# Performance work log

Hardware: AMD Instinct MI355X
Metric: run time of the kernel (lower is better)

Reference implementation:

```python
import jax, jax.numpy as jnp
import numpy as np

N_NODES = 100000
N_EDGES = 1600000
F_IN = 128
HID = 64
HORIZON = 100
NUM_TARGETS = 3


def setup_inputs() -> dict:
    key = jax.random.key(0)
    ks = jax.random.split(key, 7)
    x = jax.random.normal(ks[0], (N_NODES, F_IN), dtype=jnp.float32)
    edge_index = jax.random.randint(ks[1], (2, N_EDGES), 0, N_NODES, dtype=jnp.int64)
    s = 1.0 / np.sqrt(F_IN)
    W_l = jax.random.uniform(ks[2], (HID, F_IN), jnp.float32, -s, s)
    b_l = jax.random.uniform(ks[3], (HID,), jnp.float32, -s, s)
    W_r = jax.random.uniform(ks[4], (HID, F_IN), jnp.float32, -s, s)
    s2 = 1.0 / np.sqrt(HID)
    W_out = jax.random.uniform(ks[5], (NUM_TARGETS * HORIZON, HID), jnp.float32, -s2, s2)
    b_out = jax.random.uniform(ks[6], (NUM_TARGETS * HORIZON,), jnp.float32, -s2, s2)
    return {"x": x, "edge_index": edge_index, "W_l": W_l, "b_l": b_l,
            "W_r": W_r, "W_out": W_out, "b_out": b_out}


def reference(x, edge_index, W_l, b_l, W_r, W_out, b_out):
    n = x.shape[0]
    src, dst = edge_index[0], edge_index[1]
    # gather neighbor features and mean-aggregate per destination node
    msgs = x[src]  # [E, F_IN]
    agg = jax.ops.segment_sum(msgs, dst, num_segments=n)  # [N, F_IN]
    cnt = jax.ops.segment_sum(jnp.ones((edge_index.shape[1],), x.dtype), dst, num_segments=n)
    mean = agg / jnp.maximum(cnt, 1.0)[:, None]
    # SAGEConv: lin_l(aggregated) + lin_r(root), bias only on lin_l
    h = jnp.einsum('nf,hf->nh', mean, W_l) + b_l + jnp.einsum('nf,hf->nh', x, W_r)
    h = jax.nn.relu(h)
    out = jnp.einsum('nh,oh->no', h, W_out) + b_out  # [N, NUM_TARGETS*HORIZON]
    return out.reshape(-1, HORIZON)
```

## Files before the change

### kernel.cpp

```cpp
#include <hip/hip_runtime.h>

#define N_NODES 100000
#define F_IN 128
#define HID 64
#define OUT_F 300
#define WO_ROWS 320
#define NBKT 782
#define ECAP 2688
#define PART_BLOCKS 256
#define GEMM_BLOCKS 196
#define SORT_CAP 6400

typedef short bf8 __attribute__((ext_vector_type(8)));
typedef float f32x4 __attribute__((ext_vector_type(4)));

__device__ inline unsigned short f2bf(float f) {
    unsigned u = __builtin_bit_cast(unsigned, f);
    u += 0x7fff + ((u >> 16) & 1);
    return (unsigned short)(u >> 16);
}
__device__ inline float b2f(unsigned short h) {
    return __builtin_bit_cast(float, (unsigned)h << 16);
}

__global__ void k_prep(const float* __restrict__ Wl, const float* __restrict__ Wr,
                       const float* __restrict__ Wout,
                       unsigned short* __restrict__ Wc, unsigned short* __restrict__ Wo,
                       int* __restrict__ gcur) {
    int idx = blockIdx.x * blockDim.x + threadIdx.x;
    if (idx < 128 * 128) {
        int c = idx >> 7, k = idx & 127;
        float v = (c < HID) ? Wl[c * F_IN + k] : Wr[(c - HID) * F_IN + k];
        Wc[idx] = f2bf(v);
    } else if (idx < 128 * 128 + WO_ROWS * HID) {
        int j = idx - 128 * 128;
        int o = j >> 6, k = j & 63;
        Wo[j] = (o < OUT_F) ? f2bf(Wout[o * HID + k]) : (unsigned short)0;
    } else {
        int b = idx - 128 * 128 - WO_ROWS * HID;
        if (b < NBKT) gcur[b] = 0;
    }
}

__global__ __launch_bounds__(512) void k_pg(const int* __restrict__ ei,
                                            int* __restrict__ gcur,
                                            unsigned* __restrict__ pedges, int nE,
                                            const float* __restrict__ x,
                                            const unsigned short* __restrict__ Wc,
                                            unsigned short* __restrict__ yz) {
    if (blockIdx.x < PART_BLOCKS) {
        __shared__ unsigned sorted[SORT_CAP];
        __shared__ int hcnt[1024], hoff[1024], hcur[1024];
        __shared__ int wpre[8];
        const int tid = threadIdx.x, lane = tid & 63, wid = tid >> 6;
        const int per = (nE + PART_BLOCKS - 1) / PART_BLOCKS;
        const int e0 = blockIdx.x * per;
        const int e1 = min(e0 + per, nE);
        for (int cb = e0; cb < e1; cb += SORT_CAP) {
            const int cnt = min(SORT_CAP, e1 - cb);
            hcnt[tid * 2] = 0; hcnt[tid * 2 + 1] = 0;
            __syncthreads();
            for (int i = tid; i < cnt; i += 512)
                atomicAdd(&hcnt[ei[nE + cb + i] >> 7], 1);
            __syncthreads();
            int c0 = hcnt[tid * 2], c1 = hcnt[tid * 2 + 1];
            int tsum = c0 + c1;
            int s = tsum;
#pragma unroll
            for (int d = 1; d < 64; d <<= 1) { int t = __shfl_up(s, d, 64); if (lane >= d) s += t; }
            if (lane == 63) wpre[wid] = s;
            __syncthreads();
            if (tid == 0) { int run = 0; for (int w = 0; w < 8; ++w) { int t = wpre[w]; wpre[w] = run; run += t; } }
            __syncthreads();
            int excl = wpre[wid] + (s - tsum);
            hoff[tid * 2 + 0] = excl;       hcur[tid * 2 + 0] = excl;
            hoff[tid * 2 + 1] = excl + c0;  hcur[tid * 2 + 1] = excl + c0;
            __syncthreads();
            for (int i = tid; i < cnt; i += 512) {
                int src = ei[cb + i];
                int dst = ei[nE + cb + i];
                unsigned pk = ((unsigned)src << 7) | (unsigned)(dst & 127);
                int p = atomicAdd(&hcur[dst >> 7], 1);
                sorted[p] = pk;
            }
            __syncthreads();
            for (int b = tid; b < NBKT; b += 512) {
                int c = hcnt[b];
                if (c > 0) {
                    int gp = atomicAdd(&gcur[b], c);
                    unsigned* dst = pedges + (size_t)b * ECAP + gp;
                    int off = hoff[b];
                    for (int i = 0; i < c; ++i) dst[i] = sorted[off + i];
                }
            }
            __syncthreads();
        }
    } else {
        const int wv = threadIdx.x >> 6;
        const int nb = (blockIdx.x - PART_BLOCKS) * 512 + wv * 64;
        if (nb >= N_NODES) return;
        const int lane = threadIdx.x & 63;
        const int lm = lane & 15, lk = lane >> 4;

        f32x4 acc[4][8];
#pragma unroll
        for (int a = 0; a < 4; ++a)
#pragma unroll
            for (int b = 0; b < 8; ++b) acc[a][b] = f32x4{0.f, 0.f, 0.f, 0.f};

#pragma unroll
        for (int kt = 0; kt < 4; ++kt) {
            const int ko = kt * 32 + lk * 8;
            bf8 af[4], bw[8];
#pragma unroll
            for (int mt = 0; mt < 4; ++mt) {
                int row = nb + mt * 16 + lm;
                if (row >= N_NODES) row = N_NODES - 1;
                const float* xp = x + (size_t)row * F_IN + ko;
                float4 v0 = *(const float4*)xp;
                float4 v1 = *(const float4*)(xp + 4);
                bf8 t;
                t[0] = (short)f2bf(v0.x); t[1] = (short)f2bf(v0.y);
                t[2] = (short)f2bf(v0.z); t[3] = (short)f2bf(v0.w);
                t[4] = (short)f2bf(v1.x); t[5] = (short)f2bf(v1.y);
                t[6] = (short)f2bf(v1.z); t[7] = (short)f2bf(v1.w);
                af[mt] = t;
            }
#pragma unroll
            for (int nt = 0; nt < 8; ++nt)
                bw[nt] = *reinterpret_cast<const bf8*>(Wc + (nt * 16 + lm) * 128 + ko);
#pragma unroll
            for (int mt = 0; mt < 4; ++mt)
#pragma unroll
                for (int nt = 0; nt < 8; ++nt)
                    acc[mt][nt] = __builtin_amdgcn_mfma_f32_16x16x32_bf16(af[mt], bw[nt], acc[mt][nt], 0, 0, 0);
        }
#pragma unroll
        for (int mt = 0; mt < 4; ++mt)
#pragma unroll
            for (int r = 0; r < 4; ++r) {
                int node = nb + mt * 16 + lk * 4 + r;
                if (node < N_NODES) {
#pragma unroll
                    for (int nt = 0; nt < 8; ++nt)
                        yz[(size_t)node * 128 + nt * 16 + lm] = f2bf(acc[mt][nt][r]);
                }
            }
    }
}

#define LOAD4(e) (*(const uint2*)(yz + (size_t)(e) * 128 + f4))
#define ACC(sv0, sv1, sv2, sv3, u) \
    sv0 += b2f(u.x & 0xffff); sv1 += b2f(u.x >> 16); \
    sv2 += b2f(u.y & 0xffff); sv3 += b2f(u.y >> 16);
__global__ __launch_bounds__(512) void k_agg3(const unsigned short* __restrict__ yz,
                                              const unsigned* __restrict__ pedges,
                                              const int* __restrict__ gcur,
                                              const float* __restrict__ bl,
                                              unsigned short* __restrict__ h) {
    __shared__ unsigned esrc[ECAP];
    __shared__ int hcnt[128], hoff[128], hcur[128];
    const int tid = threadIdx.x, lane = tid & 63, wv = tid >> 6;
    const int bkt = blockIdx.x;
    int cnt = gcur[bkt]; if (cnt > ECAP) cnt = ECAP;
    const size_t base = (size_t)bkt * ECAP;
    if (tid < 128) hcnt[tid] = 0;
    __syncthreads();
    for (int i = tid; i < cnt; i += 512)
        atomicAdd(&hcnt[pedges[base + i] & 127], 1);
    __syncthreads();
    if (tid < 64) {
        int a = hcnt[2 * tid], b = hcnt[2 * tid + 1];
        int s = a + b;
#pragma unroll
        for (int d = 1; d < 64; d <<= 1) { int t = __shfl_up(s, d, 64); if (lane >= d) s += t; }
        int ex = s - (a + b);
        hoff[2 * tid] = ex;     hcur[2 * tid] = ex;
        hoff[2 * tid + 1] = ex + a; hcur[2 * tid + 1] = ex + a;
    }
    __syncthreads();
    for (int i = tid; i < cnt; i += 512) {
        unsigned e = pedges[base + i];
        int p = atomicAdd(&hcur[e & 127], 1);
        esrc[p] = e >> 7;
    }
    __syncthreads();
    const int q = lane >> 4;
    const int f4 = (lane & 15) * 4;
    float4 blv = *(const float4*)(bl + f4);
    for (int lp = 0; lp < 8; ++lp) {
        const int locA = wv * 16 + 2 * lp, locB = locA + 1;
        const int nodeA = bkt * 128 + locA, nodeB = nodeA + 1;
        const int stA = hoff[locA], dgA = hcnt[locA];
        const int stB = hoff[locB], dgB = hcnt[locB];
        float a0 = 0.f, a1 = 0.f, a2 = 0.f, a3 = 0.f;
        float b0 = 0.f, b1 = 0.f, b2 = 0.f, b3 = 0.f;
        int jA = 0, jB = 0;
        while (jA + 8 <= dgA && jB + 8 <= dgB) {
            unsigned eA0 = esrc[stA + jA + q],  eA1 = esrc[stA + jA + 4 + q];
            unsigned eB0 = esrc[stB + jB + q],  eB1 = esrc[stB + jB + 4 + q];
            uint2 uA0 = LOAD4(eA0), uA1 = LOAD4(eA1);
            uint2 uB0 = LOAD4(eB0), uB1 = LOAD4(eB1);
            ACC(a0, a1, a2, a3, uA0) ACC(a0, a1, a2, a3, uA1)
            ACC(b0, b1, b2, b3, uB0) ACC(b0, b1, b2, b3, uB1)
            jA += 8; jB += 8;
        }
        while (jA + 8 <= dgA) {
            unsigned eA0 = esrc[stA + jA + q], eA1 = esrc[stA + jA + 4 + q];
            uint2 uA0 = LOAD4(eA0), uA1 = LOAD4(eA1);
            ACC(a0, a1, a2, a3, uA0) ACC(a0, a1, a2, a3, uA1)
            jA += 8;
        }
        while (jB + 8 <= dgB) {
            unsigned eB0 = esrc[stB + jB + q], eB1 = esrc[stB + jB + 4 + q];
            uint2 uB0 = LOAD4(eB0), uB1 = LOAD4(eB1);
            ACC(b0, b1, b2, b3, uB0) ACC(b0, b1, b2, b3, uB1)
            jB += 8;
        }
        if (jA + 4 <= dgA) {
            uint2 u = LOAD4(esrc[stA + jA + q]);
            ACC(a0, a1, a2, a3, u)
            jA += 4;
        }
        if (jB + 4 <= dgB) {
            uint2 u = LOAD4(esrc[stB + jB + q]);
            ACC(b0, b1, b2, b3, u)
            jB += 4;
        }
        if (q < dgA - jA) {
            uint2 u = LOAD4(esrc[stA + jA + q]);
            ACC(a0, a1, a2, a3, u)
        }
        if (q < dgB - jB) {
            uint2 u = LOAD4(esrc[stB + jB + q]);
            ACC(b0, b1, b2, b3, u)
        }
        a0 += __shfl_xor(a0, 16); a0 += __shfl_xor(a0, 32);
        a1 += __shfl_xor(a1, 16); a1 += __shfl_xor(a1, 32);
        a2 += __shfl_xor(a2, 16); a2 += __shfl_xor(a2, 32);
        a3 += __shfl_xor(a3, 16); a3 += __shfl_xor(a3, 32);
        b0 += __shfl_xor(b0, 16); b0 += __shfl_xor(b0, 32);
        b1 += __shfl_xor(b1, 16); b1 += __shfl_xor(b1, 32);
        b2 += __shfl_xor(b2, 16); b2 += __shfl_xor(b2, 32);
        b3 += __shfl_xor(b3, 16); b3 += __shfl_xor(b3, 32);
        if (q == 0) {
            if (nodeA < N_NODES) {
                float inv = 1.0f / fmaxf((float)dgA, 1.0f);
                uint2 zu = *(const uint2*)(yz + (size_t)nodeA * 128 + HID + f4);
                float v0 = a0 * inv + b2f(zu.x & 0xffff) + blv.x;
                float v1 = a1 * inv + b2f(zu.x >> 16)    + blv.y;
                float v2 = a2 * inv + b2f(zu.y & 0xffff) + blv.z;
                float v3 = a3 * inv + b2f(zu.y >> 16)    + blv.w;
                uint2 hv;
                hv.x = (unsigned)f2bf(fmaxf(v0, 0.f)) | ((unsigned)f2bf(fmaxf(v1, 0.f)) << 16);
                hv.y = (unsigned)f2bf(fmaxf(v2, 0.f)) | ((unsigned)f2bf(fmaxf(v3, 0.f)) << 16);
                *(uint2*)(h + (size_t)nodeA * HID + f4) = hv;
            }
            if (nodeB < N_NODES) {
                float inv = 1.0f / fmaxf((float)dgB, 1.0f);
                uint2 zu = *(const uint2*)(yz + (size_t)nodeB * 128 + HID + f4);
                float v0 = b0 * inv + b2f(zu.x & 0xffff) + blv.x;
                float v1 = b1 * inv + b2f(zu.x >> 16)    + blv.y;
                float v2 = b2 * inv + b2f(zu.y & 0xffff) + blv.z;
                float v3 = b3 * inv + b2f(zu.y >> 16)    + blv.w;
                uint2 hv;
                hv.x = (unsigned)f2bf(fmaxf(v0, 0.f)) | ((unsigned)f2bf(fmaxf(v1, 0.f)) << 16);
                hv.y = (unsigned)f2bf(fmaxf(v2, 0.f)) | ((unsigned)f2bf(fmaxf(v3, 0.f)) << 16);
                *(uint2*)(h + (size_t)nodeB * HID + f4) = hv;
            }
        }
    }
}

__global__ __launch_bounds__(256) void k_fused3(
    const unsigned short* __restrict__ h, const unsigned short* __restrict__ Wo,
    const float* __restrict__ bout, float* __restrict__ out) {

    const int tid = threadIdx.x;
    const int lane = tid & 63;
    const int wv = tid >> 6;
    const int lm = lane & 15, lk = lane >> 4;
    const int node_g = blockIdx.x * 64 + wv * 16 + lm;
    int row = (node_g < N_NODES) ? node_g : (N_NODES - 1);

    bf8 ah[2];
#pragma unroll
    for (int k2 = 0; k2 < 2; ++k2)
        ah[k2] = *reinterpret_cast<const bf8*>(h + (size_t)row * HID + k2 * 32 + lk * 8);

    for (int g = 0; g < 5; ++g) {
        f32x4 acc2[4];
#pragma unroll
        for (int b = 0; b < 4; ++b) acc2[b] = f32x4{0.f, 0.f, 0.f, 0.f};
#pragma unroll
        for (int k2 = 0; k2 < 2; ++k2) {
            bf8 bw[4];
#pragma unroll
            for (int nt = 0; nt < 4; ++nt)
                bw[nt] = *reinterpret_cast<const bf8*>(
                    Wo + (size_t)((g * 4 + nt) * 16 + lm) * HID + k2 * 32 + lk * 8);
#pragma unroll
            for (int nt = 0; nt < 4; ++nt)
                acc2[nt] = __builtin_amdgcn_mfma_f32_16x16x32_bf16(bw[nt], ah[k2], acc2[nt], 0, 0, 0);
        }
#pragma unroll
        for (int nt = 0; nt < 4; ++nt) {
            int ob = (g * 4 + nt) * 16 + lk * 4;
            if (ob < OUT_F && node_g < N_NODES) {
                float4 bo = *(const float4*)(bout + ob);
                float4 v;
                v.x = acc2[nt][0] + bo.x;
                v.y = acc2[nt][1] + bo.y;
                v.z = acc2[nt][2] + bo.z;
                v.w = acc2[nt][3] + bo.w;
                *(float4*)(out + (size_t)node_g * OUT_F + ob) = v;
            }
        }
    }
}

extern "C" void kernel_launch(void* const* d_in, const int* in_sizes, int n_in,
                              void* d_out, int out_size, void* d_ws, size_t ws_size,
                              hipStream_t stream) {
    const float* x    = (const float*)d_in[0];
    const int*   ei   = (const int*)d_in[1];
    const float* Wl   = (const float*)d_in[2];
    const float* bl   = (const float*)d_in[3];
    const float* Wr   = (const float*)d_in[4];
    const float* Wout = (const float*)d_in[5];
    const float* bout = (const float*)d_in[6];
    float* out = (float*)d_out;

    int nE = in_sizes[1] / 2;

    unsigned short* yz = (unsigned short*)d_ws;
    unsigned short* h  = yz + (size_t)N_NODES * 128;
    unsigned* pedges = (unsigned*)(h + (size_t)N_NODES * HID);
    int* gcur  = (int*)(pedges + (size_t)NBKT * ECAP);
    unsigned short* Wc = (unsigned short*)(gcur + NBKT);
    unsigned short* Wo = Wc + 128 * 128;

    int prep_n = 128 * 128 + WO_ROWS * HID + NBKT;
    k_prep<<<(prep_n + 255) / 256, 256, 0, stream>>>(Wl, Wr, Wout, Wc, Wo, gcur);
    k_pg<<<PART_BLOCKS + GEMM_BLOCKS, 512, 0, stream>>>(ei, gcur, pedges, nE, x, Wc, yz);
    k_agg3<<<NBKT, 512, 0, stream>>>(yz, pedges, gcur, bl, h);
    k_fused3<<<(N_NODES + 63) / 64, 256, 0, stream>>>(h, Wo, bout, out);
}
```

Before: 135.3 us.

## Single-pass register-held edge partition and transposed MFMA for packed stores

The partition phase now uses more blocks and processes each block's edge range in one pass, keeping src/dst in registers (EPT per thread) instead of re-reading them across a chunked loop. Any overflow edges go straight to global buckets via per-edge atomics. The GEMM swaps MFMA operands so each lane holds four consecutive output features of one node, allowing packed 8-byte bf16 stores instead of scalar 2-byte stores. It adds register pressure and relies on per-block edge counts mostly fitting in EPT*512.

Result: slower. 143.1 us (+5.8%).

```diff
diff --git a/kernel.cpp b/kernel.cpp
--- a/kernel.cpp
+++ b/kernel.cpp
@@ -7,9 +7,10 @@
 #define WO_ROWS 320
 #define NBKT 782
 #define ECAP 2688
-#define PART_BLOCKS 256
+#define PART_BLOCKS 384
 #define GEMM_BLOCKS 196
-#define SORT_CAP 6400
+#define SORT_CAP 4224
+#define EPT 9
 
 typedef short bf8 __attribute__((ext_vector_type(8)));
 typedef float f32x4 __attribute__((ext_vector_type(4)));
@@ -55,45 +56,56 @@
         const int tid = threadIdx.x, lane = tid & 63, wid = tid >> 6;
         const int per = (nE + PART_BLOCKS - 1) / PART_BLOCKS;
         const int e0 = blockIdx.x * per;
-        const int e1 = min(e0 + per, nE);
-        for (int cb = e0; cb < e1; cb += SORT_CAP) {
-            const int cnt = min(SORT_CAP, e1 - cb);
-            hcnt[tid * 2] = 0; hcnt[tid * 2 + 1] = 0;
-            __syncthreads();
-            for (int i = tid; i < cnt; i += 512)
-                atomicAdd(&hcnt[ei[nE + cb + i] >> 7], 1);
-            __syncthreads();
-            int c0 = hcnt[tid * 2], c1 = hcnt[tid * 2 + 1];
-            int tsum = c0 + c1;
-            int s = tsum;
-#pragma unroll
-            for (int d = 1; d < 64; d <<= 1) { int t = __shfl_up(s, d, 64); if (lane >= d) s += t; }
-            if (lane == 63) wpre[wid] = s;
-            __syncthreads();
-            if (tid == 0) { int run = 0; for (int w = 0; w < 8; ++w) { int t = wpre[w]; wpre[w] = run; run += t; } }
-            __syncthreads();
-            int excl = wpre[wid] + (s - tsum);
-            hoff[tid * 2 + 0] = excl;       hcur[tid * 2 + 0] = excl;
-            hoff[tid * 2 + 1] = excl + c0;  hcur[tid * 2 + 1] = excl + c0;
-            __syncthreads();
-            for (int i = tid; i < cnt; i += 512) {
-                int src = ei[cb + i];
-                int dst = ei[nE + cb + i];
-                unsigned pk = ((unsigned)src << 7) | (unsigned)(dst & 127);
-                int p = atomicAdd(&hcur[dst >> 7], 1);
-                sorted[p] = pk;
-            }
-            __syncthreads();
-            for (int b = tid; b < NBKT; b += 512) {
-                int c = hcnt[b];
-                if (c > 0) {
-                    int gp = atomicAdd(&gcur[b], c);
-                    unsigned* dst = pedges + (size_t)b * ECAP + gp;
-                    int off = hoff[b];
-                    for (int i = 0; i < c; ++i) dst[i] = sorted[off + i];
-                }
-            }
-            __syncthreads();
+        const int cnt = min(per, nE - e0);
+        int mysrc[EPT], mydst[EPT];
+        hcnt[tid * 2] = 0; hcnt[tid * 2 + 1] = 0;
+        __syncthreads();
+#pragma unroll
+        for (int m = 0; m < EPT; ++m) {
+            int i = m * 512 + tid;
+            if (i < cnt) {
+                mydst[m] = ei[nE + e0 + i];
+                mysrc[m] = ei[e0 + i];
+                atomicAdd(&hcnt[mydst[m] >> 7], 1);
+            }
+        }
+        for (int i = EPT * 512 + tid; i < cnt; i += 512) {
+            int src = ei[e0 + i], dst = ei[nE + e0 + i];
+            int b = dst >> 7;
+            int p = atomicAdd(&gcur[b], 1);
+            if (p < ECAP) pedges[(size_t)b * ECAP + p] = ((unsigned)src << 7) | (unsigned)(dst & 127);
+        }
+        __syncthreads();
+        int c0 = hcnt[tid * 2], c1 = hcnt[tid * 2 + 1];
+        int tsum = c0 + c1;
+        int s = tsum;
+#pragma unroll
+        for (int d = 1; d < 64; d <<= 1) { int t = __shfl_up(s, d, 64); if (lane >= d) s += t; }
+        if (lane == 63) wpre[wid] = s;
+        __syncthreads();
+        if (tid == 0) { int run = 0; for (int w = 0; w < 8; ++w) { int t = wpre[w]; wpre[w] = run; run += t; } }
+        __syncthreads();
+        int excl = wpre[wid] + (s - tsum);
+        hoff[tid * 2 + 0] = excl;       hcur[tid * 2 + 0] = excl;
+        hoff[tid * 2 + 1] = excl + c0;  hcur[tid * 2 + 1] = excl + c0;
+        __syncthreads();
+#pragma unroll
+        for (int m = 0; m < EPT; ++m) {
+            int i = m * 512 + tid;
+            if (i < cnt) {
+                int p = atomicAdd(&hcur[mydst[m] >> 7], 1);
+                sorted[p] = ((unsigned)mysrc[m] << 7) | (unsigned)(mydst[m] & 127);
+            }
+        }
+        __syncthreads();
+        for (int b = tid; b < NBKT; b += 512) {
+            int c = hcnt[b];
+            if (c > 0) {
+                int gp = atomicAdd(&gcur[b], c);
+                unsigned* dst = pedges + (size_t)b * ECAP + gp;
+                int off = hoff[b];
+                for (int i = 0; i < c; ++i) dst[i] = sorted[off + i];
+            }
         }
     } else {
         const int wv = threadIdx.x >> 6;
@@ -133,19 +145,21 @@
             for (int mt = 0; mt < 4; ++mt)
 #pragma unroll
                 for (int nt = 0; nt < 8; ++nt)
-                    acc[mt][nt] = __builtin_amdgcn_mfma_f32_16x16x32_bf16(af[mt], bw[nt], acc[mt][nt], 0, 0, 0);
-        }
-#pragma unroll
-        for (int mt = 0; mt < 4; ++mt)
-#pragma unroll
-            for (int r = 0; r < 4; ++r) {
-                int node = nb + mt * 16 + lk * 4 + r;
-                if (node < N_NODES) {
-#pragma unroll
-                    for (int nt = 0; nt < 8; ++nt)
-                        yz[(size_t)node * 128 + nt * 16 + lm] = f2bf(acc[mt][nt][r]);
+                    acc[mt][nt] = __builtin_amdgcn_mfma_f32_16x16x32_bf16(bw[nt], af[mt], acc[mt][nt], 0, 0, 0);
+        }
+#pragma unroll
+        for (int mt = 0; mt < 4; ++mt) {
+            int node = nb + mt * 16 + lm;
+            if (node < N_NODES) {
+#pragma unroll
+                for (int nt = 0; nt < 8; ++nt) {
+                    uint2 v;
+                    v.x = (unsigned)f2bf(acc[mt][nt][0]) | ((unsigned)f2bf(acc[mt][nt][1]) << 16);
+                    v.y = (unsigned)f2bf(acc[mt][nt][2]) | ((unsigned)f2bf(acc[mt][nt][3]) << 16);
+                    *(uint2*)(yz + (size_t)node * 128 + nt * 16 + lk * 4) = v;
                 }
             }
+        }
     }
 }
 
```
